# Kernel optimization log

Measured on AMD Instinct MI355X. Metric: run time of the kernel, lower is better.

The kernel has to match this reference:

```python
import jax, jax.numpy as jnp
import numpy as np

N, N_FEAT, F1, F2, F3, N_Z = 4096, 512, 256, 128, 64, 16
SLOPE = 0.2
NEG = -9e16


def _xavier(key, shape):
    std = (2.0 / (shape[0] + shape[1])) ** 0.5
    return jax.random.normal(key, shape, dtype=jnp.float32) * std


def setup_inputs() -> dict:
    key = jax.random.key(0)
    ks = jax.random.split(key, 20)
    x = jax.random.normal(ks[0], (N, N_FEAT), dtype=jnp.float32)
    adj = jax.random.randint(ks[1], (N, N), 0, 2, dtype=jnp.int32)
    dims = [N_FEAT, F1, F2, F3, N_Z, F3, F2, F1, N_FEAT]
    inp = {"x": x, "adj": adj}
    for i in range(8):
        fi, fo = dims[i], dims[i + 1]
        inp[f"w{i+1}"] = _xavier(ks[2 + 2 * i], (fi, fo))
        inp[f"a{i+1}"] = _xavier(ks[3 + 2 * i], (2 * fo, 1))
    return inp


def _gat(x, adj_pos, w, a):
    h = x @ w                               # [N, f_out]
    f = h.shape[1]
    src = h @ a[:f]                         # [N, 1]
    tgt = h @ a[f:]                         # [N, 1]
    e = jax.nn.leaky_relu(src + tgt.T, SLOPE)  # [N, N] broadcast score sum
    e = jnp.where(adj_pos, e, NEG)
    attn = jax.nn.softmax(e, axis=-1)
    return attn @ h                          # [N, f_out]


def reference(x, adj, w1, a1, w2, a2, w3, a3, w4, a4, w5, a5, w6, a6, w7, a7, w8, a8):
    adj_pos = adj > 0
    h1 = _gat(x, adj_pos, w1, a1)
    h2 = _gat(h1, adj_pos, w2, a2)
    h3 = _gat(h2, adj_pos, w3, a3)
    h4 = _gat(h3, adj_pos, w4, a4)
    h5 = _gat(h4, adj_pos, w5, a5)
    h6 = _gat(h5, adj_pos, w6, a6)
    h7 = _gat(h6, adj_pos, w7, a7)
    x_bar = _gat(h7, adj_pos, w8, a8)
    return (x_bar, h1, h2, h3, h4)
```

## Files before the change

kernel.cpp:

```cpp
#include <hip/hip_runtime.h>
#include <hip/hip_bf16.h>


#define NROWS 4096
#define TMC 12.0f

typedef __attribute__((ext_vector_type(8))) short v8s;
typedef __attribute__((ext_vector_type(4))) float v4f;

__device__ inline unsigned short f2bf(float x) {
  union { float f; unsigned u; } v; v.f = x;
  unsigned r = v.u + 0x7fffu + ((v.u >> 16) & 1u);
  return (unsigned short)(r >> 16);
}

__global__ void pack_adj(const int* __restrict__ adj, unsigned long long* __restrict__ bits) {
  int row = blockIdx.x;
  int lane = threadIdx.x & 63, wave = threadIdx.x >> 6;
  for (int w = wave; w < 64; w += 4) {
    unsigned long long m = __ballot(adj[(size_t)row * NROWS + w * 64 + lane] > 0);
    if (lane == 0) bits[row * 64 + w] = m;
  }
}

struct WTArgs { const float* src[8]; unsigned short* dst[8]; int K[8]; int F[8]; };
__global__ void transpose_w(WTArgs A) {
  int z = blockIdx.z;
  const float* in = A.src[z];
  unsigned short* out = A.dst[z];
  int R = A.K[z], C = A.F[z];
  __shared__ unsigned short tile[32][33];
  int c0 = blockIdx.x * 32, r0 = blockIdx.y * 32;
  if (c0 >= C || r0 >= R) return;
#pragma unroll
  for (int dy = 0; dy < 32; dy += 8) {
    int r = r0 + threadIdx.y + dy, c = c0 + threadIdx.x;
    if (r < R && c < C) tile[threadIdx.y + dy][threadIdx.x] = f2bf(in[(size_t)r * C + c]);
  }
  __syncthreads();
#pragma unroll
  for (int dy = 0; dy < 32; dy += 8) {
    int c = c0 + threadIdx.y + dy, r = r0 + threadIdx.x;
    if (r < R && c < C) out[(size_t)c * R + r] = tile[threadIdx.x][threadIdx.y + dy];
  }
}

__global__ __launch_bounds__(128) void gemm_xw(const float* __restrict__ A,
                                               const unsigned short* __restrict__ BT,
                                               float* __restrict__ C,
                                               unsigned short* __restrict__ HTt,
                                               int K, int Nf) {
  __shared__ unsigned short zone[64 * 36];
  int lane = threadIdx.x & 63, wave = threadIdx.x >> 6;
  int quad = lane >> 4, l16 = lane & 15;
  int row0 = blockIdx.x * 32 + wave * 16;
  int col0 = blockIdx.y * 64;
  int nf = Nf - col0; nf = nf > 64 ? 4 : (nf + 15) / 16;
  v4f acc[4] = {{0.f,0.f,0.f,0.f},{0.f,0.f,0.f,0.f},{0.f,0.f,0.f,0.f},{0.f,0.f,0.f,0.f}};
  for (int k0 = 0; k0 < K; k0 += 32) {
    int kk = k0 + quad * 8;
    v8s a = {0,0,0,0,0,0,0,0};
    if (kk < K) {
      float4 f0 = *(const float4*)(A + (size_t)(row0 + l16) * K + kk);
      float4 f1 = *(const float4*)(A + (size_t)(row0 + l16) * K + kk + 4);
      union { v8s s; __hip_bfloat162 h[4]; } ua;
      ua.h[0] = __float22bfloat162_rn(make_float2(f0.x, f0.y));
      ua.h[1] = __float22bfloat162_rn(make_float2(f0.z, f0.w));
      ua.h[2] = __float22bfloat162_rn(make_float2(f1.x, f1.y));
      ua.h[3] = __float22bfloat162_rn(make_float2(f1.z, f1.w));
      a = ua.s;
    }
    for (int t = 0; t < nf; t++) {
      v8s b = {0,0,0,0,0,0,0,0};
      if (kk < K) b = *(const v8s*)(BT + (size_t)(col0 + t * 16 + l16) * K + kk);
      acc[t] = __builtin_amdgcn_mfma_f32_16x16x32_bf16(a, b, acc[t], 0, 0, 0);
    }
  }
  for (int t = 0; t < nf; t++) {
#pragma unroll
    for (int r = 0; r < 4; r++) {
      float v = acc[t][r];
      C[(size_t)(row0 + quad * 4 + r) * Nf + col0 + t * 16 + l16] = v;
      zone[(t * 16 + l16) * 36 + wave * 16 + quad * 4 + r] = f2bf(v);
    }
  }
  __syncthreads();
  unsigned* dst = (unsigned*)(HTt + (size_t)(blockIdx.x) * Nf * 32 + (size_t)col0 * 32);
  const unsigned* zsrc = (const unsigned*)zone;
  int total = nf * 256;
  for (int idx = threadIdx.x; idx < total; idx += 128) {
    int f = idx >> 4, jp = idx & 15;
    dst[idx] = zsrc[f * 18 + jp];
  }
}

__global__ void gemv_srctgt(const float* __restrict__ H, const float* __restrict__ a,
                            float* __restrict__ src, float* __restrict__ Ev,
                            float* __restrict__ Gv, int f) {
  int row = blockIdx.x * 4 + (threadIdx.x >> 6);
  int lane = threadIdx.x & 63;
  float s = 0.f, t = 0.f;
  for (int k = lane; k < f; k += 64) {
    float h = H[(size_t)row * f + k];
    s += h * a[k];
    t += h * a[f + k];
  }
#pragma unroll
  for (int off = 32; off; off >>= 1) { s += __shfl_down(s, off); t += __shfl_down(t, off); }
  if (lane == 0) {
    src[row] = s;
    Ev[row] = __expf(t - TMC);
    Gv[row] = __expf(0.2f * (t - TMC));
  }
}

__global__ void pass1b(const unsigned long long* __restrict__ bits, const float* __restrict__ src,
                       const float* __restrict__ Ev, const float* __restrict__ Gv,
                       float* __restrict__ Av, float* __restrict__ Bv) {
  int row = blockIdx.x * 4 + (threadIdx.x >> 6);
  int lane = threadIdx.x & 63;
  float sp = src[row] + TMC;
  float m = sp > 0.f ? sp : 0.2f * sp;
  float P = __expf(sp - m), Q = __expf(0.2f * sp - m);
  const unsigned long long* brow = bits + (size_t)row * 64;
  float lsum = 0.f;
  for (int k = 0; k < 64; k++) {
    unsigned long long w = brow[k];
    float v = fmaxf(P * Ev[k * 64 + lane], Q * Gv[k * 64 + lane]);
    lsum += ((w >> lane) & 1ull) ? v : 0.f;
  }
#pragma unroll
  for (int off = 32; off; off >>= 1) lsum += __shfl_xor(lsum, off);
  if (lane == 0) {
    float inv = 1.0f / lsum;
    Av[row] = P * inv;
    Bv[row] = Q * inv;
  }
}

template<int NF>
__global__ __launch_bounds__(256) void pass2f(const unsigned* __restrict__ adjW,
                                              const float* __restrict__ Av,
                                              const float* __restrict__ Bv,
                                              const float* __restrict__ Ev,
                                              const float* __restrict__ Gv,
                                              const unsigned short* __restrict__ HTt,
                                              float* __restrict__ out,
                                              float* __restrict__ part, int F, int js) {
  const int W = NF * 16, Wp = W + 4;
  __shared__ float zone[32 * Wp];
  int lane = threadIdx.x & 63, wave = threadIdx.x >> 6;
  int quad = lane >> 4, l16 = lane & 15;
  int i0 = blockIdx.x * 32;
  int fc0 = blockIdx.y * W;
  const size_t F32 = (size_t)F * 32;
  int jrange = NROWS / js;
  int jlen = jrange / 4;
  int jstart = blockIdx.z * jrange + wave * jlen;

  float Ai[2], Bi[2];
  const unsigned* arow[2];
#pragma unroll
  for (int ni = 0; ni < 2; ni++) {
    int i = i0 + ni * 16 + l16;
    Ai[ni] = Av[i]; Bi[ni] = Bv[i];
    arow[ni] = adjW + (size_t)i * 128;
  }
  v4f acc[2][NF];
#pragma unroll
  for (int ni = 0; ni < 2; ni++)
#pragma unroll
    for (int t = 0; t < NF; t++) acc[ni][t] = (v4f){0.f, 0.f, 0.f, 0.f};

  for (int j0 = jstart; j0 < jstart + jlen; j0 += 32) {
    int jb = j0 + quad * 8;
    float4 e0 = *(const float4*)(Ev + jb), e1 = *(const float4*)(Ev + jb + 4);
    float4 g0 = *(const float4*)(Gv + jb), g1 = *(const float4*)(Gv + jb + 4);
    float ev[8] = {e0.x, e0.y, e0.z, e0.w, e1.x, e1.y, e1.z, e1.w};
    float gv[8] = {g0.x, g0.y, g0.z, g0.w, g1.x, g1.y, g1.z, g1.w};
    const unsigned short* bp = HTt + (size_t)(j0 >> 5) * F32 + (size_t)(fc0 + l16) * 32 + quad * 8;
    v8s bfr[NF];
#pragma unroll
    for (int t = 0; t < NF; t++) bfr[t] = *(const v8s*)(bp + t * 512);
#pragma unroll
    for (int ni = 0; ni < 2; ni++) {
      unsigned bb = arow[ni][j0 >> 5] >> (quad * 8);
      float w[8];
#pragma unroll
      for (int jj = 0; jj < 8; jj++) {
        float v = fmaxf(Ai[ni] * ev[jj], Bi[ni] * gv[jj]);
        int msk = ((int)(bb << (31 - jj))) >> 31;
        w[jj] = __int_as_float(msk & __float_as_int(v));
      }
      union { v8s s; __hip_bfloat162 h[4]; } ua;
#pragma unroll
      for (int p = 0; p < 4; p++)
        ua.h[p] = __float22bfloat162_rn(make_float2(w[2 * p], w[2 * p + 1]));
#pragma unroll
      for (int t = 0; t < NF; t++)
        acc[ni][t] = __builtin_amdgcn_mfma_f32_16x16x32_bf16(ua.s, bfr[t], acc[ni][t], 0, 0, 0);
    }
  }

  for (int w = 0; w < 4; w++) {
    if (wave == w) {
#pragma unroll
      for (int ni = 0; ni < 2; ni++)
#pragma unroll
        for (int t = 0; t < NF; t++)
#pragma unroll
          for (int r = 0; r < 4; r++) {
            int idx = (ni * 16 + quad * 4 + r) * Wp + t * 16 + l16;
            if (w == 0) zone[idx] = acc[ni][t][r];
            else        zone[idx] += acc[ni][t][r];
          }
    }
    __syncthreads();
  }
  float* dst = (blockIdx.z == 0) ? out : part + (size_t)(blockIdx.z - 1) * NROWS * F;
  for (int idx = threadIdx.x; idx < 32 * W; idx += 256) {
    int rrow = idx / W, ccol = idx - rrow * W;
    dst[(size_t)(i0 + rrow) * F + fc0 + ccol] = zone[rrow * Wp + ccol];
  }
}

__global__ void reduce_add(const float* __restrict__ part, float* __restrict__ out, int n,
                           int nslab) {
  int i = blockIdx.x * 256 + threadIdx.x;
  if (i < n) {
    float s = out[i];
    for (int z = 0; z < nslab; z++) s += part[(size_t)z * n + i];
    out[i] = s;
  }
}

static void launch_pass2(int NF, dim3 grid, const unsigned* adjW, const float* Av, const float* Bv,
                         const float* Ev, const float* Gv, const unsigned short* HTt, float* out,
                         float* part, int F, int js, hipStream_t stream) {
  switch (NF) {
    case 8: pass2f<8><<<grid, 256, 0, stream>>>(adjW, Av, Bv, Ev, Gv, HTt, out, part, F, js); break;
    case 4: pass2f<4><<<grid, 256, 0, stream>>>(adjW, Av, Bv, Ev, Gv, HTt, out, part, F, js); break;
    default: pass2f<1><<<grid, 256, 0, stream>>>(adjW, Av, Bv, Ev, Gv, HTt, out, part, F, js); break;
  }
}

extern "C" void kernel_launch(void* const* d_in, const int* in_sizes, int n_in,
                              void* d_out, int out_size, void* d_ws, size_t ws_size,
                              hipStream_t stream) {
  static const int fin[8]  = {512, 256, 128, 64, 16, 64, 128, 256};
  static const int fout[8] = {256, 128, 64, 16, 64, 128, 256, 512};

  const float* x = (const float*)d_in[0];
  const int* adj = (const int*)d_in[1];
  char* ws = (char*)d_ws;
  unsigned long long* bits = (unsigned long long*)(ws);
  unsigned short* WTall = (unsigned short*)(ws + (2u << 20));
  float* H            = (float*)(ws + (6u << 20));
  unsigned short* HTt = (unsigned short*)(ws + (14u << 20));
  float* srcv = (float*)(ws + (19u << 20));
  float* Av   = (float*)(ws + (19u << 20) + 49152);
  float* Bv   = (float*)(ws + (19u << 20) + 65536);
  float* Ev   = (float*)(ws + (19u << 20) + 81920);
  float* Gv   = (float*)(ws + (19u << 20) + 98304);
  float* o5   = (float*)(ws + (20u << 20));
  float* o6   = (float*)(ws + (21u << 20));
  float* o7   = (float*)(ws + (23u << 20));
  float* part = H;

  float* outp = (float*)d_out;
  float* xbar = outp;
  float* h1 = outp + (size_t)NROWS * 512;
  float* h2 = h1 + (size_t)NROWS * 256;
  float* h3 = h2 + (size_t)NROWS * 128;
  float* h4 = h3 + (size_t)NROWS * 64;

  float* louts[8] = {h1, h2, h3, h4, o5, o6, o7, xbar};
  const float* lins[8] = {x, h1, h2, h3, h4, o5, o6, o7};

  unsigned short* WT[8];
  { size_t off = 0;
    for (int t = 0; t < 8; t++) { WT[t] = WTall + off; off += (size_t)fin[t] * fout[t]; } }

  pack_adj<<<dim3(4096), dim3(256), 0, stream>>>(adj, bits);

  WTArgs wa;
  for (int t = 0; t < 8; t++) {
    wa.src[t] = (const float*)d_in[2 + 2 * t];
    wa.dst[t] = WT[t];
    wa.K[t] = fin[t];
    wa.F[t] = fout[t];
  }
  transpose_w<<<dim3(16, 16, 8), dim3(32, 8), 0, stream>>>(wa);

  for (int t = 0; t < 8; t++) {
    int K = fin[t], F = fout[t];
    const float* At = (const float*)d_in[3 + 2 * t];
    const float* Xin = lins[t];
    float* Ot = louts[t];

    int NF = F >= 128 ? 8 : (F >= 64 ? 4 : 1);
    int fc = F / (16 * NF);
    int js = (F == 512) ? 1 : (F == 256 ? 2 : 4);

    gemm_xw<<<dim3(128, (F + 63) / 64), dim3(128), 0, stream>>>(Xin, WT[t], H, HTt, K, F);
    gemv_srctgt<<<dim3(1024), dim3(256), 0, stream>>>(H, At, srcv, Ev, Gv, F);
    pass1b<<<dim3(1024), dim3(256), 0, stream>>>(bits, srcv, Ev, Gv, Av, Bv);
    launch_pass2(NF, dim3(128, fc, js), (const unsigned*)bits, Av, Bv, Ev, Gv, HTt, Ot, part, F,
                 js, stream);
    if (js > 1)
      reduce_add<<<dim3((NROWS * F + 255) / 256), dim3(256), 0, stream>>>(part, Ot, NROWS * F,
                                                                          js - 1);
  }
}
```

Measured before the change: 574.8 us.

## Switch attention-weight path to packed fp16 math with fp16 MFMA

The attention pass now stores H transposed as fp16 instead of bf16, precomputes scaled fp16 copies of the exp(tgt) vectors, and builds the masked weights with packed half2 multiply and max before feeding fp16 MFMA. The adjacency words are loaded 128 columns at a time, and the inner loop is unrolled over four 32-column chunks. The goal is to cut per-element VALU work and conversion cost in the weight-building stage. It risks fp16 overflow or underflow in H and in the weights, which the 2^14 and 2^4 scale factors are meant to guard against.

```diff
diff --git a/kernel.cpp b/kernel.cpp
--- a/kernel.cpp
+++ b/kernel.cpp
@@ -1,11 +1,14 @@
 #include <hip/hip_runtime.h>
 #include <hip/hip_bf16.h>
+#include <hip/hip_fp16.h>
 
 
 #define NROWS 4096
 #define TMC 12.0f
 
 typedef __attribute__((ext_vector_type(8))) short v8s;
+typedef __attribute__((ext_vector_type(8))) _Float16 v8h;
+typedef __attribute__((ext_vector_type(2))) _Float16 h2v;
 typedef __attribute__((ext_vector_type(4))) float v4f;
 
 __device__ inline unsigned short f2bf(float x) {
@@ -81,7 +84,8 @@
     for (int r = 0; r < 4; r++) {
       float v = acc[t][r];
       C[(size_t)(row0 + quad * 4 + r) * Nf + col0 + t * 16 + l16] = v;
-      zone[(t * 16 + l16) * 36 + wave * 16 + quad * 4 + r] = f2bf(v);
+      union { _Float16 h; unsigned short s; } cv; cv.h = (_Float16)v;
+      zone[(t * 16 + l16) * 36 + wave * 16 + quad * 4 + r] = cv.s;
     }
   }
   __syncthreads();
@@ -96,7 +100,8 @@
 
 __global__ void gemv_srctgt(const float* __restrict__ H, const float* __restrict__ a,
                             float* __restrict__ src, float* __restrict__ Ev,
-                            float* __restrict__ Gv, int f) {
+                            float* __restrict__ Gv, unsigned short* __restrict__ Ev16,
+                            unsigned short* __restrict__ Gv16, int f) {
   int row = blockIdx.x * 4 + (threadIdx.x >> 6);
   int lane = threadIdx.x & 63;
   float s = 0.f, t = 0.f;
@@ -109,8 +114,13 @@
   for (int off = 32; off; off >>= 1) { s += __shfl_down(s, off); t += __shfl_down(t, off); }
   if (lane == 0) {
     src[row] = s;
-    Ev[row] = __expf(t - TMC);
-    Gv[row] = __expf(0.2f * (t - TMC));
+    float ev = __expf(t - TMC), gv = __expf(0.2f * (t - TMC));
+    Ev[row] = ev; Gv[row] = gv;
+    union { _Float16 h; unsigned short u; } ce, cg;
+    ce.h = (_Float16)(ev * 16384.f);
+    cg.h = (_Float16)(gv * 16.f);
+    Ev16[row] = ce.u;
+    Gv16[row] = cg.u;
   }
 }
 
@@ -142,8 +152,8 @@
 __global__ __launch_bounds__(256) void pass2f(const unsigned* __restrict__ adjW,
                                               const float* __restrict__ Av,
                                               const float* __restrict__ Bv,
-                                              const float* __restrict__ Ev,
-                                              const float* __restrict__ Gv,
+                                              const unsigned short* __restrict__ Ev16,
+                                              const unsigned short* __restrict__ Gv16,
                                               const unsigned short* __restrict__ HTt,
                                               float* __restrict__ out,
                                               float* __restrict__ part, int F, int js) {
@@ -158,12 +168,15 @@
   int jlen = jrange / 4;
   int jstart = blockIdx.z * jrange + wave * jlen;
 
-  float Ai[2], Bi[2];
+  h2v Ai2[2], Bi2[2];
   const unsigned* arow[2];
 #pragma unroll
   for (int ni = 0; ni < 2; ni++) {
     int i = i0 + ni * 16 + l16;
-    Ai[ni] = Av[i]; Bi[ni] = Bv[i];
+    _Float16 ai = (_Float16)(Av[i] * 0x1p-14f);
+    _Float16 bi = (_Float16)(Bv[i] * 0x1p-4f);
+    Ai2[ni] = (h2v){ai, ai};
+    Bi2[ni] = (h2v){bi, bi};
     arow[ni] = adjW + (size_t)i * 128;
   }
   v4f acc[2][NF];
@@ -172,33 +185,40 @@
 #pragma unroll
     for (int t = 0; t < NF; t++) acc[ni][t] = (v4f){0.f, 0.f, 0.f, 0.f};
 
-  for (int j0 = jstart; j0 < jstart + jlen; j0 += 32) {
-    int jb = j0 + quad * 8;
-    float4 e0 = *(const float4*)(Ev + jb), e1 = *(const float4*)(Ev + jb + 4);
-    float4 g0 = *(const float4*)(Gv + jb), g1 = *(const float4*)(Gv + jb + 4);
-    float ev[8] = {e0.x, e0.y, e0.z, e0.w, e1.x, e1.y, e1.z, e1.w};
-    float gv[8] = {g0.x, g0.y, g0.z, g0.w, g1.x, g1.y, g1.z, g1.w};
-    const unsigned short* bp = HTt + (size_t)(j0 >> 5) * F32 + (size_t)(fc0 + l16) * 32 + quad * 8;
-    v8s bfr[NF];
-#pragma unroll
-    for (int t = 0; t < NF; t++) bfr[t] = *(const v8s*)(bp + t * 512);
-#pragma unroll
-    for (int ni = 0; ni < 2; ni++) {
-      unsigned bb = arow[ni][j0 >> 5] >> (quad * 8);
-      float w[8];
-#pragma unroll
-      for (int jj = 0; jj < 8; jj++) {
-        float v = fmaxf(Ai[ni] * ev[jj], Bi[ni] * gv[jj]);
-        int msk = ((int)(bb << (31 - jj))) >> 31;
-        w[jj] = __int_as_float(msk & __float_as_int(v));
+  for (int j0 = jstart; j0 < jstart + jlen; j0 += 128) {
+    uint4 aw[2];
+    aw[0] = *(const uint4*)(arow[0] + (j0 >> 5));
+    aw[1] = *(const uint4*)(arow[1] + (j0 >> 5));
+    unsigned awa[2][4] = {{aw[0].x, aw[0].y, aw[0].z, aw[0].w},
+                          {aw[1].x, aw[1].y, aw[1].z, aw[1].w}};
+#pragma unroll
+    for (int u = 0; u < 4; u++) {
+      int ju = j0 + u * 32;
+      int jb = ju + quad * 8;
+      union { v8s s; h2v h2[4]; } ue, ug;
+      ue.s = *(const v8s*)(Ev16 + jb);
+      ug.s = *(const v8s*)(Gv16 + jb);
+      const unsigned short* bp =
+          HTt + (size_t)(ju >> 5) * F32 + (size_t)(fc0 + l16) * 32 + quad * 8;
+      union { v8s s; v8h h; } bfr[NF];
+#pragma unroll
+      for (int t = 0; t < NF; t++) bfr[t].s = *(const v8s*)(bp + t * 512);
+#pragma unroll
+      for (int ni = 0; ni < 2; ni++) {
+        unsigned bb = awa[ni][u] >> (quad * 8);
+        union { v8h h; unsigned u32[4]; } ua;
+#pragma unroll
+        for (int p = 0; p < 4; p++) {
+          h2v w2 = __builtin_elementwise_max(Ai2[ni] * ue.h2[p], Bi2[ni] * ug.h2[p]);
+          unsigned msk = (((bb >> (2 * p)) & 1u) ? 0x0000FFFFu : 0u)
+                       | (((bb >> (2 * p + 1)) & 1u) ? 0xFFFF0000u : 0u);
+          union { h2v h2; unsigned u; } tw; tw.h2 = w2;
+          ua.u32[p] = tw.u & msk;
+        }
+#pragma unroll
+        for (int t = 0; t < NF; t++)
+          acc[ni][t] = __builtin_amdgcn_mfma_f32_16x16x32_f16(ua.h, bfr[t].h, acc[ni][t], 0, 0, 0);
       }
-      union { v8s s; __hip_bfloat162 h[4]; } ua;
-#pragma unroll
-      for (int p = 0; p < 4; p++)
-        ua.h[p] = __float22bfloat162_rn(make_float2(w[2 * p], w[2 * p + 1]));
-#pragma unroll
-      for (int t = 0; t < NF; t++)
-        acc[ni][t] = __builtin_amdgcn_mfma_f32_16x16x32_bf16(ua.s, bfr[t], acc[ni][t], 0, 0, 0);
     }
   }
 
@@ -235,12 +255,16 @@
 }
 
 static void launch_pass2(int NF, dim3 grid, const unsigned* adjW, const float* Av, const float* Bv,
-                         const float* Ev, const float* Gv, const unsigned short* HTt, float* out,
-                         float* part, int F, int js, hipStream_t stream) {
+                         const unsigned short* Ev16, const unsigned short* Gv16,
+                         const unsigned short* HTt, float* out, float* part, int F, int js,
+                         hipStream_t stream) {
   switch (NF) {
-    case 8: pass2f<8><<<grid, 256, 0, stream>>>(adjW, Av, Bv, Ev, Gv, HTt, out, part, F, js); break;
-    case 4: pass2f<4><<<grid, 256, 0, stream>>>(adjW, Av, Bv, Ev, Gv, HTt, out, part, F, js); break;
-    default: pass2f<1><<<grid, 256, 0, stream>>>(adjW, Av, Bv, Ev, Gv, HTt, out, part, F, js); break;
+    case 8: pass2f<8><<<grid, 256, 0, stream>>>(adjW, Av, Bv, Ev16, Gv16, HTt, out, part, F, js);
+            break;
+    case 4: pass2f<4><<<grid, 256, 0, stream>>>(adjW, Av, Bv, Ev16, Gv16, HTt, out, part, F, js);
+            break;
+    default: pass2f<1><<<grid, 256, 0, stream>>>(adjW, Av, Bv, Ev16, Gv16, HTt, out, part, F, js);
+            break;
   }
 }
 
@@ -257,14 +281,16 @@
   unsigned short* WTall = (unsigned short*)(ws + (2u << 20));
   float* H            = (float*)(ws + (6u << 20));
   unsigned short* HTt = (unsigned short*)(ws + (14u << 20));
-  float* srcv = (float*)(ws + (19u << 20));
-  float* Av   = (float*)(ws + (19u << 20) + 49152);
-  float* Bv   = (float*)(ws + (19u << 20) + 65536);
-  float* Ev   = (float*)(ws + (19u << 20) + 81920);
-  float* Gv   = (float*)(ws + (19u << 20) + 98304);
-  float* o5   = (float*)(ws + (20u << 20));
-  float* o6   = (float*)(ws + (21u << 20));
-  float* o7   = (float*)(ws + (23u << 20));
+  float* srcv  = (float*)(ws + (19u << 20));
+  float* Av    = (float*)(ws + (19u << 20) + 49152);
+  float* Bv    = (float*)(ws + (19u << 20) + 65536);
+  float* Ev    = (float*)(ws + (19u << 20) + 81920);
+  float* Gv    = (float*)(ws + (19u << 20) + 98304);
+  unsigned short* Ev16 = (unsigned short*)(ws + (19u << 20) + 114688);
+  unsigned short* Gv16 = (unsigned short*)(ws + (19u << 20) + 122880);
+  float* o5    = (float*)(ws + (20u << 20));
+  float* o6    = (float*)(ws + (21u << 20));
+  float* o7    = (float*)(ws + (23u << 20));
   float* part = H;
 
   float* outp = (float*)d_out;
@@ -303,10 +329,10 @@
     int js = (F == 512) ? 1 : (F == 256 ? 2 : 4);
 
     gemm_xw<<<dim3(128, (F + 63) / 64), dim3(128), 0, stream>>>(Xin, WT[t], H, HTt, K, F);
-    gemv_srctgt<<<dim3(1024), dim3(256), 0, stream>>>(H, At, srcv, Ev, Gv, F);
+    gemv_srctgt<<<dim3(1024), dim3(256), 0, stream>>>(H, At, srcv, Ev, Gv, Ev16, Gv16, F);
     pass1b<<<dim3(1024), dim3(256), 0, stream>>>(bits, srcv, Ev, Gv, Av, Bv);
-    launch_pass2(NF, dim3(128, fc, js), (const unsigned*)bits, Av, Bv, Ev, Gv, HTt, Ot, part, F,
-                 js, stream);
+    launch_pass2(NF, dim3(128, fc, js), (const unsigned*)bits, Av, Bv, Ev16, Gv16, HTt, Ot, part,
+                 F, js, stream);
     if (js > 1)
       reduce_add<<<dim3((NROWS * F + 255) / 256), dim3(256), 0, stream>>>(part, Ot, NROWS * F,
                                                                           js - 1);
```

After: 533.3 us. -7.2%, faster.
